# Kernel optimization log

Measured on AMD Instinct MI355X. Metric: run time of the kernel, lower is better.

The kernel has to match this reference:

```python
import jax, jax.numpy as jnp
import numpy as np

EMBED_DIM = 2048
N_HEADS = 16
N_KV_HEADS = 4
HEAD_DIM = EMBED_DIM // N_HEADS  # 128
NUM_REP = N_HEADS // N_KV_HEADS  # 4
BATCH = 4
SEQLEN = 2048


def setup_inputs() -> dict:
    key = jax.random.key(0)
    kx, kq, kk, kv, ko = jax.random.split(key, 5)
    x = jax.random.normal(kx, (BATCH, SEQLEN, EMBED_DIM), dtype=jnp.float32)
    # Real RoPE table (theta=10000), shape (seqlen, head_dim//2)
    inv_freq = 1.0 / (10000.0 ** (jnp.arange(0, HEAD_DIM, 2, dtype=jnp.float32) / HEAD_DIM))
    t = jnp.arange(SEQLEN, dtype=jnp.float32)
    ang = jnp.outer(t, inv_freq)  # (S, hd/2)
    freqs_cos = jnp.cos(ang)
    freqs_sin = jnp.sin(ang)
    std = 0.02
    wq = jax.random.normal(kq, (EMBED_DIM, N_HEADS * HEAD_DIM), dtype=jnp.float32) * std
    wk = jax.random.normal(kk, (EMBED_DIM, N_KV_HEADS * HEAD_DIM), dtype=jnp.float32) * std
    wv = jax.random.normal(kv, (EMBED_DIM, N_KV_HEADS * HEAD_DIM), dtype=jnp.float32) * std
    wo = jax.random.normal(ko, (N_HEADS * HEAD_DIM, EMBED_DIM), dtype=jnp.float32) * std
    return {"x": x, "freqs_cos": freqs_cos, "freqs_sin": freqs_sin,
            "wq": wq, "wk": wk, "wv": wv, "wo": wo}


def _apply_rope(xh, cos, sin):
    # xh: (b, s, h, hd); cos/sin: (s, hd/2) -> broadcast (1, s, 1, hd/2)
    b, s, h, hd = xh.shape
    xr = xh.reshape(b, s, h, hd // 2, 2)
    x0, x1 = xr[..., 0], xr[..., 1]  # real/imag of complex pairs
    c = cos[None, :, None, :]
    sn = sin[None, :, None, :]
    o0 = x0 * c - x1 * sn
    o1 = x0 * sn + x1 * c
    return jnp.stack([o0, o1], axis=-1).reshape(b, s, h, hd)


def reference(x, freqs_cos, freqs_sin, wq, wk, wv, wo):
    bs, s, _ = x.shape
    xq = (x @ wq).reshape(bs, s, N_HEADS, HEAD_DIM)
    xk = (x @ wk).reshape(bs, s, N_KV_HEADS, HEAD_DIM)
    xv = (x @ wv).reshape(bs, s, N_KV_HEADS, HEAD_DIM)
    xq = _apply_rope(xq, freqs_cos, freqs_sin)
    xk = _apply_rope(xk, freqs_cos, freqs_sin)
    # repeat_kv (GQA): interleave-repeat kv heads to match query heads
    keys = jnp.repeat(xk, NUM_REP, axis=2)    # (b, s, H, hd)
    values = jnp.repeat(xv, NUM_REP, axis=2)
    scale = 1.0 / jnp.sqrt(jnp.float32(HEAD_DIM))
    # SDPA, non-causal
    scores = jnp.einsum('bqhd,bkhd->bhqk', xq, keys) * scale
    probs = jax.nn.softmax(scores, axis=-1)
    out = jnp.einsum('bhqk,bkhd->bqhd', probs, values)
    out = out.reshape(bs, s, N_HEADS * HEAD_DIM)
    return out @ wo
```

## Files before the change

kernel.cpp:

```cpp
#include <hip/hip_runtime.h>
#include <stdint.h>


typedef unsigned short u16;
typedef __bf16 bf16x8 __attribute__((ext_vector_type(8)));
typedef float  f32x4  __attribute__((ext_vector_type(4)));
typedef unsigned int u32x2 __attribute__((ext_vector_type(2)));

#define GLOAD16(gp, lp)                                                        \
  __builtin_amdgcn_global_load_lds(                                            \
      (const __attribute__((address_space(1))) void*)(gp),                     \
      (__attribute__((address_space(3))) void*)(lp), 16, 0, 0)

__device__ __forceinline__ u16 f2b(float f) {
  union { float f; uint32_t u; } v; v.f = f;
  uint32_t r = v.u + 0x7FFFu + ((v.u >> 16) & 1u);
  return (u16)(r >> 16);
}
__device__ __forceinline__ float b2f(u16 h) {
  union { uint32_t u; float f; } v; v.u = ((uint32_t)h) << 16;
  return v.f;
}
__device__ __forceinline__ uint2 pack4(float a, float b, float c, float d) {
  uint2 r;
  asm("v_cvt_pk_bf16_f32 %0, %1, %2" : "=v"(r.x) : "v"(a), "v"(b));
  asm("v_cvt_pk_bf16_f32 %0, %1, %2" : "=v"(r.y) : "v"(c), "v"(d));
  return r;
}

__device__ __forceinline__ void bar_sync() {
  asm volatile("s_waitcnt lgkmcnt(0)" ::: "memory");
  __builtin_amdgcn_s_barrier();
  asm volatile("" ::: "memory");
}

__global__ __launch_bounds__(256) void cast_x_kernel(const float4* __restrict__ in,
                                                     ushort4* __restrict__ out) {
  int i = blockIdx.x * 256 + threadIdx.x;
  float4 v = in[i];
  ushort4 o;
  o.x = f2b(v.x); o.y = f2b(v.y); o.z = f2b(v.z); o.w = f2b(v.w);
  out[i] = o;
}

__global__ __launch_bounds__(256) void wtrans_kernel(const float* __restrict__ W,
                                                     u16* __restrict__ WT,
                                                     int K, int N, float scale) {
  __shared__ float t[32][33];
  int n0 = blockIdx.x * 32, k0 = blockIdx.y * 32;
  int tx = threadIdx.x, ty = threadIdx.y;
  for (int r = 0; r < 4; r++)
    t[ty + r * 8][tx] = W[(size_t)(k0 + ty + r * 8) * N + n0 + tx];
  __syncthreads();
  for (int r = 0; r < 4; r++)
    WT[(size_t)(n0 + ty + r * 8) * K + k0 + tx] = f2b(t[tx][ty + r * 8] * scale);
}

#define KSTEP(CUR, NXT, TT)                                                    \
  {                                                                            \
    asm volatile("s_waitcnt vmcnt(0)" ::: "memory");                           \
    bar_sync();                                                                \
    if ((TT) + 1 < nt) {                                                       \
      const size_t k0 = (size_t)((TT) + 1) * 32;                               \
      GLOAD16(Ag + k0, &As[NXT][ldst]);                                        \
      GLOAD16(Ag + k0 + (size_t)16 * K, &As[NXT][ldst + 512]);                 \
      GLOAD16(Bg + k0, &Bs[NXT][ldst]);                                        \
      GLOAD16(Bg + k0 + (size_t)16 * K, &Bs[NXT][ldst + 512]);                 \
    }                                                                          \
    bf16x8 af[4], bf[4];                                                       \
    for (int i = 0; i < 4; i++)                                                \
      af[i] = *(const bf16x8*)&As[CUR][wm * 32 + i * 512 + lrd];               \
    for (int i = 0; i < 4; i++)                                                \
      bf[i] = *(const bf16x8*)&Bs[CUR][wn * 32 + i * 512 + lrd];               \
    __builtin_amdgcn_s_setprio(1);                                             \
    for (int mi = 0; mi < 4; mi++)                                             \
      for (int ni = 0; ni < 4; ni++)                                           \
        acc[mi][ni] = __builtin_amdgcn_mfma_f32_16x16x32_bf16(                 \
            af[mi], bf[ni], acc[mi][ni], 0, 0, 0);                             \
    __builtin_amdgcn_s_setprio(0);                                             \
  }

template <bool BF16OUT>
__global__ __launch_bounds__(256) void gemm_bt_kernel(const u16* __restrict__ A,
                                                      const u16* __restrict__ BT,
                                                      void* __restrict__ Cv,
                                                      int K, int N) {
  __shared__ u16 As[2][64 * 64];
  __shared__ u16 Bs[2][64 * 64];
  const int tid = threadIdx.x;
  const int wave = tid >> 6, lane = tid & 63;
  const int quad = lane >> 4, l16 = lane & 15;
  const int wm = (wave >> 1) * 64, wn = (wave & 1) * 64;

  const int nbx = gridDim.x;
  const int nwg = nbx * gridDim.y;
  const int d = blockIdx.x + blockIdx.y * nbx;
  const int w = (d & 7) * (nwg >> 3) + (d >> 3);
  const size_t m0 = (size_t)(w / nbx) * 128, n0 = (size_t)(w % nbx) * 128;

  f32x4 acc[4][4] = {};
  const int srow = wave * 32 + ((lane >> 3) << 1) + ((lane >> 2) & 1);
  const int tcol = ((lane & 3) ^ ((lane >> 3) & 3)) * 8;
  const u16* Ag = A + (m0 + srow) * (size_t)K + tcol;
  const u16* Bg = BT + (n0 + srow) * (size_t)K + tcol;
  const int ldst = wave * 1024;
  const int lrd = (l16 >> 1) * 64 + (l16 & 1) * 32 +
                  ((quad ^ ((l16 >> 1) & 3)) << 3);
  const int nt = K >> 5;

  GLOAD16(Ag, &As[0][ldst]);
  GLOAD16(Ag + (size_t)16 * K, &As[0][ldst + 512]);
  GLOAD16(Bg, &Bs[0][ldst]);
  GLOAD16(Bg + (size_t)16 * K, &Bs[0][ldst + 512]);

  for (int t = 0; t < nt; t += 2) {
    KSTEP(0, 1, t);
    KSTEP(1, 0, t + 1);
  }

  for (int mi = 0; mi < 4; mi++)
    for (int ni = 0; ni < 4; ni++)
      for (int r = 0; r < 4; r++) {
        size_t row = m0 + wm + mi * 16 + quad * 4 + r;
        size_t col = n0 + wn + ni * 16 + l16;
        if (BF16OUT) ((u16*)Cv)[row * N + col] = f2b(acc[mi][ni][r]);
        else         ((float*)Cv)[row * N + col] = acc[mi][ni][r];
      }
}

__global__ __launch_bounds__(256) void rope_kernel(u16* __restrict__ QKV,
                                                   const float* __restrict__ cs,
                                                   const float* __restrict__ sn) {
  int tid = blockIdx.x * 256 + threadIdx.x;
  int row = tid / 1280;
  int p = tid - row * 1280;
  int s = row & 2047;
  int head = p >> 6, i = p & 63;
  u16* ptr = QKV + (size_t)row * 3072 + head * 128 + i * 2;
  unsigned int v = *(unsigned int*)ptr;
  float x0 = b2f((u16)(v & 0xffff)), x1 = b2f((u16)(v >> 16));
  float c = cs[s * 64 + i], ss = sn[s * 64 + i];
  u16 o0 = f2b(x0 * c - x1 * ss);
  u16 o1 = f2b(x0 * ss + x1 * c);
  *(unsigned int*)ptr = (unsigned int)o0 | ((unsigned int)o1 << 16);
}

__global__ __launch_bounds__(256) void vtrans_kernel(const u16* __restrict__ QKV,
                                                     u16* __restrict__ Vt) {
  __shared__ u16 t[32][33];
  int b = blockIdx.z >> 2, hk = blockIdx.z & 3;
  int s0 = blockIdx.x * 32, d0 = blockIdx.y * 32;
  int tx = threadIdx.x, ty = threadIdx.y;
  const u16* src = QKV + (size_t)(b * 2048 + s0) * 3072 + 2560 + hk * 128 + d0;
  for (int r = 0; r < 4; r++)
    t[ty + r * 8][tx] = src[(size_t)(ty + r * 8) * 3072 + tx];
  __syncthreads();
  u16* dst = Vt + ((size_t)((b * 4 + hk) * 128 + d0)) * 2048 + s0;
  for (int r = 0; r < 4; r++)
    dst[(size_t)(ty + r * 8) * 2048 + tx] = t[tx][ty + r * 8];
}

__global__ __launch_bounds__(256, 2) void attn_kernel(const u16* __restrict__ QKV,
                                                      const u16* __restrict__ Vt,
                                                      u16* __restrict__ AO) {
  __shared__ u16 KP[128 * 128];
  __shared__ u16 Vls[128 * 128];
  const int tid = threadIdx.x;
  const int wave = tid >> 6, lane = tid & 63;
  const int quad = lane >> 4, l16 = lane & 15;
  const int d0s = blockIdx.x + 16 * (blockIdx.y + 16 * blockIdx.z);
  const int w0 = (d0s & 7) * 128 + (d0s >> 3);
  const int qt = w0 & 15, h = (w0 >> 4) & 15, b = w0 >> 8;
  const int hk = h >> 2;
  const int sw = l16 & 7;

  bf16x8 qf[2][4];
  {
    const u16* Qb = QKV + (size_t)(b * 2048 + qt * 128 + wave * 32) * 3072 + h * 128;
    for (int qb = 0; qb < 2; qb++)
      for (int ki = 0; ki < 4; ki++)
        qf[qb][ki] = *(const bf16x8*)(Qb + (size_t)(qb * 16 + l16) * 3072 + ki * 32 + quad * 8);
  }
  f32x4 o[8][2] = {};
  float m_[2] = {-1e30f, -1e30f}, l_[2] = {0.f, 0.f};

  const u16* Kg0 = QKV + 2048 + hk * 128;
  const u16* Vg0 = Vt + (size_t)((b * 4 + hk) * 128) * 2048;
  const int r4 = lane >> 4, c16 = lane & 15;

  auto stageK = [&](int t) {
    const u16* Kg = Kg0 + (size_t)(b * 2048 + t * 128) * 3072;
    for (int i = 0; i < 8; i++) {
      int grp = i * 4 + wave;
      int row = grp * 4 + r4;
      int ch = c16 ^ (row & 7);
      GLOAD16(Kg + (size_t)row * 3072 + ch * 8, &KP[grp * 512]);
    }
  };
  auto stageV = [&](int t) {
    const u16* Vg = Vg0 + t * 128;
    for (int i = 0; i < 8; i++) {
      int grp = i * 4 + wave;
      int row = grp * 4 + r4;
      int ch = c16 ^ (row & 7);
      GLOAD16(Vg + (size_t)row * 2048 + ch * 8, &Vls[grp * 512]);
    }
  };

  stageK(0);
  stageV(0);
  __syncthreads();

  for (int kt = 0; kt < 16; kt++) {
    if (kt > 0) stageV(kt);

    f32x4 s[8][2];
    for (int kb = 0; kb < 8; kb++) {
      bf16x8 kf[4];
      int a0 = (kb * 16 + l16) * 128 + ((quad ^ sw) << 3);
      for (int ki = 0; ki < 4; ki++)
        kf[ki] = *(const bf16x8*)&KP[a0 ^ (ki * 32)];
      __builtin_amdgcn_s_setprio(1);
      for (int qb = 0; qb < 2; qb++) {
        f32x4 a = {0.f, 0.f, 0.f, 0.f};
        for (int ki = 0; ki < 4; ki++)
          a = __builtin_amdgcn_mfma_f32_16x16x32_bf16(kf[ki], qf[qb][ki], a, 0, 0, 0);
        s[kb][qb] = a;
      }
      __builtin_amdgcn_s_setprio(0);
    }

    bar_sync();
    if (kt < 15) stageK(kt + 1);

    bf16x8 pf[2][4];
    float alch[2];
    for (int qb = 0; qb < 2; qb++) {
      float mk[8];
#pragma unroll
      for (int kb = 0; kb < 8; kb++)
        mk[kb] = fmaxf(fmaxf(s[kb][qb][0], s[kb][qb][1]),
                       fmaxf(s[kb][qb][2], s[kb][qb][3]));
      float mx = fmaxf(fmaxf(fmaxf(mk[0], mk[1]), fmaxf(mk[2], mk[3])),
                       fmaxf(fmaxf(mk[4], mk[5]), fmaxf(mk[6], mk[7])));
      mx = fmaxf(mx, __shfl_xor(mx, 16, 64));
      mx = fmaxf(mx, __shfl_xor(mx, 32, 64));
      float mn = m_[qb], al = 1.0f;
      if (!__all(mx <= m_[qb] + 8.0f)) {
        mn = fmaxf(m_[qb], mx);
        al = exp2f(m_[qb] - mn);
        m_[qb] = mn;
      }
      alch[qb] = al;
      uint2 u[8];
      float rs = 0.f;
#pragma unroll
      for (int kb = 0; kb < 8; kb++) {
        float p0 = exp2f(s[kb][qb][0] - mn), p1 = exp2f(s[kb][qb][1] - mn);
        float p2 = exp2f(s[kb][qb][2] - mn), p3 = exp2f(s[kb][qb][3] - mn);
        u[kb] = pack4(p0, p1, p2, p3);
        rs += (p0 + p1) + (p2 + p3);
      }
      rs += __shfl_xor(rs, 16, 64);
      rs += __shfl_xor(rs, 32, 64);
      l_[qb] = l_[qb] * al + rs;
      const bool qo = (quad & 1) != 0;
#pragma unroll
      for (int ki = 0; ki < 4; ki++) {
        u32x2 r1 = __builtin_amdgcn_permlane32_swap(u[2 * ki].x, u[2 * ki + 1].x, false, false);
        u32x2 r2 = __builtin_amdgcn_permlane32_swap(u[2 * ki].y, u[2 * ki + 1].y, false, false);
        uint32_t t1b = (uint32_t)__shfl_xor((int)r1[1], 16, 64);
        uint32_t t1a = (uint32_t)__shfl_xor((int)r1[0], 16, 64);
        uint32_t t2b = (uint32_t)__shfl_xor((int)r2[1], 16, 64);
        uint32_t t2a = (uint32_t)__shfl_xor((int)r2[0], 16, 64);
        uint4 d;
        d.x = qo ? t1b : (uint32_t)r1[0];
        d.y = qo ? t2b : (uint32_t)r2[0];
        d.z = qo ? (uint32_t)r1[1] : t1a;
        d.w = qo ? (uint32_t)r2[1] : t2a;
        pf[qb][ki] = *(bf16x8*)&d;
      }
    }
    if (alch[0] != 1.0f || alch[1] != 1.0f) {
#pragma unroll
      for (int db = 0; db < 8; db++) {
        o[db][0] *= alch[0];
        o[db][1] *= alch[1];
      }
    }

    if (kt == 15) asm volatile("s_waitcnt vmcnt(0)" ::: "memory");
    else          asm volatile("s_waitcnt vmcnt(8)" ::: "memory");
    bar_sync();

    for (int db = 0; db < 8; db++) {
      bf16x8 vf[4];
      int a0 = (db * 16 + l16) * 128 + ((quad ^ sw) << 3);
      for (int ki = 0; ki < 4; ki++)
        vf[ki] = *(const bf16x8*)&Vls[a0 ^ (ki * 32)];
      __builtin_amdgcn_s_setprio(1);
      for (int qb = 0; qb < 2; qb++)
        for (int ki = 0; ki < 4; ki++)
          o[db][qb] = __builtin_amdgcn_mfma_f32_16x16x32_bf16(vf[ki], pf[qb][ki], o[db][qb], 0, 0, 0);
      __builtin_amdgcn_s_setprio(0);
    }

    asm volatile("s_waitcnt vmcnt(0)" ::: "memory");
    bar_sync();
  }

  float inv[2] = {1.0f / l_[0], 1.0f / l_[1]};
  for (int qb = 0; qb < 2; qb++) {
    int rq = wave * 32 + qb * 16 + l16;
    for (int db = 0; db < 8; db++) {
      int ch = (db * 2 + (quad >> 1)) ^ sw;
      uint2 pv = pack4(o[db][qb][0] * inv[qb], o[db][qb][1] * inv[qb],
                       o[db][qb][2] * inv[qb], o[db][qb][3] * inv[qb]);
      *(uint2*)&KP[rq * 128 + (ch << 3) + (quad & 1) * 4] = pv;
    }
  }
  __syncthreads();
  u16* Ab = AO + (size_t)(b * 2048 + qt * 128) * 2048 + h * 128;
  for (int i = 0; i < 8; i++) {
    int row = i * 16 + (tid >> 4);
    int seg = tid & 15;
    int pc = seg ^ (row & 7);
    *(uint4*)(Ab + (size_t)row * 2048 + seg * 8) = *(const uint4*)&KP[row * 128 + pc * 8];
  }
}

extern "C" void kernel_launch(void* const* d_in, const int* in_sizes, int n_in,
                              void* d_out, int out_size, void* d_ws, size_t ws_size,
                              hipStream_t stream) {
  (void)in_sizes; (void)n_in; (void)out_size; (void)ws_size;
  const float* x    = (const float*)d_in[0];
  const float* fcos = (const float*)d_in[1];
  const float* fsin = (const float*)d_in[2];
  const float* wq   = (const float*)d_in[3];
  const float* wk   = (const float*)d_in[4];
  const float* wv   = (const float*)d_in[5];
  const float* wo   = (const float*)d_in[6];

  char* w = (char*)d_ws;
  u16* xb  = (u16*)w;
  u16* wT  = (u16*)(w + 33554432);
  u16* woT = (u16*)(w + 33554432 + 12582912);
  u16* QKV = (u16*)(w + 33554432 + 12582912 + 8388608);
  u16* Vt  = (u16*)(w + 33554432 + 12582912 + 8388608 + 50331648);
  u16* AO  = xb;

  const float C = 0.08838834764831845f * 1.44269504088896340f;

  cast_x_kernel<<<16384, 256, 0, stream>>>((const float4*)x, (ushort4*)xb);
  wtrans_kernel<<<dim3(64, 64), dim3(32, 8), 0, stream>>>(wq, wT, 2048, 2048, C);
  wtrans_kernel<<<dim3(16, 64), dim3(32, 8), 0, stream>>>(wk, wT + (size_t)2048 * 2048, 2048, 512, 1.0f);
  wtrans_kernel<<<dim3(16, 64), dim3(32, 8), 0, stream>>>(wv, wT + (size_t)2560 * 2048, 2048, 512, 1.0f);
  wtrans_kernel<<<dim3(64, 64), dim3(32, 8), 0, stream>>>(wo, woT, 2048, 2048, 1.0f);

  gemm_bt_kernel<true><<<dim3(24, 64), 256, 0, stream>>>(xb, wT, QKV, 2048, 3072);
  rope_kernel<<<40960, 256, 0, stream>>>(QKV, fcos, fsin);
  vtrans_kernel<<<dim3(64, 4, 16), dim3(32, 8), 0, stream>>>(QKV, Vt);
  attn_kernel<<<dim3(16, 16, 4), 256, 0, stream>>>(QKV, Vt, AO);
  gemm_bt_kernel<false><<<dim3(16, 64), 256, 0, stream>>>(AO, woT, (float*)d_out, 2048, 2048);
}
```

Measured before the change: 573.1 us.

## Triple-buffer GEMM LDS tiles and drop attention XCD block remap

The bf16 GEMM moves from two to three LDS stages. Loads for tile t+2 are issued while tile t is computed, and the wait becomes a partial vmcnt(4) instead of a full drain, so global-to-LDS latency overlaps more compute at the cost of 50% more LDS. The loop tail is hand-unrolled and assumes K/32 ≡ 1 mod 3. Separately, the attention kernel stops remapping block IDs across XCDs and uses blockIdx directly, which changes which heads and batches share each L2.

```diff
diff --git a/kernel.cpp b/kernel.cpp
--- a/kernel.cpp
+++ b/kernel.cpp
@@ -56,16 +56,17 @@
     WT[(size_t)(n0 + ty + r * 8) * K + k0 + tx] = f2b(t[tx][ty + r * 8] * scale);
 }
 
-#define KSTEP(CUR, NXT, TT)                                                    \
+#define KSTEP(CUR, TT)                                                         \
   {                                                                            \
-    asm volatile("s_waitcnt vmcnt(0)" ::: "memory");                           \
+    if ((TT) + 1 < nt) asm volatile("s_waitcnt vmcnt(4)" ::: "memory");        \
+    else               asm volatile("s_waitcnt vmcnt(0)" ::: "memory");        \
     bar_sync();                                                                \
-    if ((TT) + 1 < nt) {                                                       \
-      const size_t k0 = (size_t)((TT) + 1) * 32;                               \
-      GLOAD16(Ag + k0, &As[NXT][ldst]);                                        \
-      GLOAD16(Ag + k0 + (size_t)16 * K, &As[NXT][ldst + 512]);                 \
-      GLOAD16(Bg + k0, &Bs[NXT][ldst]);                                        \
-      GLOAD16(Bg + k0 + (size_t)16 * K, &Bs[NXT][ldst + 512]);                 \
+    if ((TT) + 2 < nt) {                                                       \
+      const size_t k0 = (size_t)((TT) + 2) * 32;                               \
+      GLOAD16(Ag + k0, &As[((CUR) + 2) % 3][ldst]);                            \
+      GLOAD16(Ag + k0 + (size_t)16 * K, &As[((CUR) + 2) % 3][ldst + 512]);     \
+      GLOAD16(Bg + k0, &Bs[((CUR) + 2) % 3][ldst]);                            \
+      GLOAD16(Bg + k0 + (size_t)16 * K, &Bs[((CUR) + 2) % 3][ldst + 512]);     \
     }                                                                          \
     bf16x8 af[4], bf[4];                                                       \
     for (int i = 0; i < 4; i++)                                                \
@@ -85,8 +86,8 @@
                                                       const u16* __restrict__ BT,
                                                       void* __restrict__ Cv,
                                                       int K, int N) {
-  __shared__ u16 As[2][64 * 64];
-  __shared__ u16 Bs[2][64 * 64];
+  __shared__ u16 As[3][64 * 64];
+  __shared__ u16 Bs[3][64 * 64];
   const int tid = threadIdx.x;
   const int wave = tid >> 6, lane = tid & 63;
   const int quad = lane >> 4, l16 = lane & 15;
@@ -112,11 +113,21 @@
   GLOAD16(Ag + (size_t)16 * K, &As[0][ldst + 512]);
   GLOAD16(Bg, &Bs[0][ldst]);
   GLOAD16(Bg + (size_t)16 * K, &Bs[0][ldst + 512]);
-
-  for (int t = 0; t < nt; t += 2) {
-    KSTEP(0, 1, t);
-    KSTEP(1, 0, t + 1);
-  }
+  GLOAD16(Ag + 32, &As[1][ldst]);
+  GLOAD16(Ag + 32 + (size_t)16 * K, &As[1][ldst + 512]);
+  GLOAD16(Bg + 32, &Bs[1][ldst]);
+  GLOAD16(Bg + 32 + (size_t)16 * K, &Bs[1][ldst + 512]);
+
+  int t = 0;
+  for (; t + 4 < nt; t += 3) {
+    KSTEP(0, t);
+    KSTEP(1, t + 1);
+    KSTEP(2, t + 2);
+  }
+  KSTEP(0, t);
+  KSTEP(1, t + 1);
+  KSTEP(2, t + 2);
+  KSTEP(0, t + 3);
 
   for (int mi = 0; mi < 4; mi++)
     for (int ni = 0; ni < 4; ni++)
@@ -168,9 +179,7 @@
   const int tid = threadIdx.x;
   const int wave = tid >> 6, lane = tid & 63;
   const int quad = lane >> 4, l16 = lane & 15;
-  const int d0s = blockIdx.x + 16 * (blockIdx.y + 16 * blockIdx.z);
-  const int w0 = (d0s & 7) * 128 + (d0s >> 3);
-  const int qt = w0 & 15, h = (w0 >> 4) & 15, b = w0 >> 8;
+  const int qt = blockIdx.x, h = blockIdx.y, b = blockIdx.z;
   const int hk = h >> 2;
   const int sw = l16 & 7;
 
```

Result: no change. 577.3 us (+0.7%).
